# Kernel optimization log

Hardware: AMD Instinct MI355X
Metric: run time of the kernel (lower is better)

The kernel has to match this reference:

```python
import jax, jax.numpy as jnp
import numpy as np

B, T, C, H = 4, 2048, 1024, 16
DH = C // H  # 64


def setup_inputs() -> dict:
    key = jax.random.key(0)
    k_x, k_qkv, k_proj = jax.random.split(key, 3)
    x = jax.random.normal(k_x, (B, T, C), dtype=jnp.float32)
    # variance-scaling (fan_in) init for linear weights, torch layout [out, in]
    qkv_w = jax.random.normal(k_qkv, (3 * C, C), dtype=jnp.float32) * (1.0 / np.sqrt(C))
    qkv_b = jnp.zeros((3 * C,), dtype=jnp.float32)
    proj_w = jax.random.normal(k_proj, (C, C), dtype=jnp.float32) * (1.0 / np.sqrt(C))
    proj_b = jnp.zeros((C,), dtype=jnp.float32)
    # causal mask, broadcastable to [B, H, T, T]
    mask = jnp.tril(jnp.ones((T, T), dtype=bool))[None, None]
    return {"x": x, "qkv_w": qkv_w, "qkv_b": qkv_b,
            "proj_w": proj_w, "proj_b": proj_b, "mask": mask}


def reference(x, qkv_w, qkv_b, proj_w, proj_b, mask):
    b, t, c = x.shape
    scale = DH ** -0.5
    qkv = (x @ qkv_w.T + qkv_b).reshape(b, t, 3, H, DH)
    qkv = jnp.transpose(qkv, (2, 0, 3, 1, 4))  # [3, B, H, T, DH]
    q, k, v = qkv[0], qkv[1], qkv[2]
    attn = jnp.einsum("bhqd,bhkd->bhqk", q, k) * scale  # [B, H, T, T]
    neg = -jnp.finfo(attn.dtype).max
    attn = jnp.where(mask, attn, neg)
    attn = jax.nn.softmax(attn, axis=-1)
    out = jnp.einsum("bhqk,bhkd->bhqd", attn, v)  # [B, H, T, DH]
    out = jnp.transpose(out, (0, 2, 1, 3)).reshape(b, t, c)
    return out @ proj_w.T + proj_b
```

## Files before the change

### kernel.cpp

```cpp
#include <hip/hip_runtime.h>
#include <hip/hip_bf16.h>
#include <stdint.h>

#define B_ 4
#define T_ 2048
#define C_ 1024
#define H_ 16
#define DH_ 64
#define M_ (B_*T_)
#define NQKV_ (3*C_)
#define K_ C_

typedef __attribute__((ext_vector_type(8))) short short8;
typedef __attribute__((ext_vector_type(4))) float f32x4;
typedef __attribute__((ext_vector_type(4))) unsigned short us4;

union BFC { __hip_bfloat16 h; unsigned short u; };
__device__ inline unsigned short f2b(float f){ BFC c; c.h = __float2bfloat16(f); return c.u; }

__device__ inline void gload_lds16(const void* g, void* l){
  __builtin_amdgcn_global_load_lds(
    (const __attribute__((address_space(1))) void*)(uintptr_t)g,
    (__attribute__((address_space(3))) void*)(uintptr_t)l,
    16, 0, 0);
}

__global__ void cvt_f32_bf16(const float* __restrict__ src,
                             __hip_bfloat16* __restrict__ dst, int n4)
{
  int i = blockIdx.x * blockDim.x + threadIdx.x;
  int stride = gridDim.x * blockDim.x;
  for (; i < n4; i += stride) {
    float4 v = reinterpret_cast<const float4*>(src)[i];
    us4 o;
    o.x = f2b(v.x); o.y = f2b(v.y); o.z = f2b(v.z); o.w = f2b(v.w);
    reinterpret_cast<us4*>(dst)[i] = o;
  }
}

__global__ __launch_bounds__(512) void gemm_bt(
    const __hip_bfloat16* __restrict__ A,
    const __hip_bfloat16* __restrict__ Bw,
    const float* __restrict__ bias,
    int mode, int nbx,
    __hip_bfloat16* __restrict__ qdst,
    __hip_bfloat16* __restrict__ kdst,
    __hip_bfloat16* __restrict__ vdst,
    float* __restrict__ fdst)
{
  __shared__ char a_lds[2][32768];
  __shared__ char b_lds[2][32768];

  const int tid = threadIdx.x;
  const int lane = tid & 63;
  const int w = tid >> 6;
  const int l15 = lane & 15;
  const int lhi = lane >> 4;
  const int wm = w >> 2, wn = w & 3;

  const int nwg = gridDim.x;
  const int q8 = nwg >> 3;
  const int lb = (blockIdx.x & 7) * q8 + (blockIdx.x >> 3);
  const int bx = lb % nbx, by = lb / nbx;
  const int row0 = by * 256;
  const int col0 = bx * 256;

  int srow[4], scol[4];
#pragma unroll
  for (int i = 0; i < 4; ++i) {
    int L = i * 8192 + tid * 16;
    int r = L >> 7;
    int cb = (L & 127) ^ ((r & 7) << 4);
    srow[i] = r;
    scol[i] = cb >> 1;
  }

  const f32x4 zf = {0.f, 0.f, 0.f, 0.f};
  f32x4 acc[8][4];
#pragma unroll
  for (int m = 0; m < 8; ++m)
#pragma unroll
    for (int n = 0; n < 4; ++n) acc[m][n] = zf;

  const short* Ag = (const short*)A;
  const short* Bg = (const short*)Bw;

#define STAGE(kt, buf)                                                          \
  do {                                                                          \
    _Pragma("unroll")                                                           \
    for (int i = 0; i < 4; ++i) {                                               \
      gload_lds16(Ag + (size_t)(row0 + srow[i]) * K_ + (kt) + scol[i],          \
                  &a_lds[buf][i * 8192 + tid * 16]);                            \
      gload_lds16(Bg + (size_t)(col0 + srow[i]) * K_ + (kt) + scol[i],          \
                  &b_lds[buf][i * 8192 + tid * 16]);                            \
    }                                                                           \
  } while (0)

  STAGE(0, 0);
  __syncthreads();

  const int NKT = K_ / 64;
  for (int ki = 0; ki < NKT; ++ki) {
    const int cur = ki & 1;
    if (ki + 1 < NKT) STAGE((ki + 1) * 64, cur ^ 1);

#pragma unroll
    for (int kf = 0; kf < 2; ++kf) {
      short8 af[8], bfr[4];
#pragma unroll
      for (int m = 0; m < 8; ++m) {
        int r = wm * 128 + m * 16 + l15;
        af[m] = *(const short8*)(&a_lds[cur][r * 128 +
                     ((kf * 64 + lhi * 16) ^ ((r & 7) << 4))]);
      }
#pragma unroll
      for (int n = 0; n < 4; ++n) {
        int r = wn * 64 + n * 16 + l15;
        bfr[n] = *(const short8*)(&b_lds[cur][r * 128 +
                     ((kf * 64 + lhi * 16) ^ ((r & 7) << 4))]);
      }
#pragma unroll
      for (int m = 0; m < 8; ++m)
#pragma unroll
        for (int n = 0; n < 4; ++n)
          acc[m][n] = __builtin_amdgcn_mfma_f32_16x16x32_bf16(af[m], bfr[n],
                                                              acc[m][n], 0, 0, 0);
    }

    __syncthreads();
  }
#undef STAGE

  if (mode == 0) {
#pragma unroll
    for (int m = 0; m < 8; ++m) {
#pragma unroll
      for (int r = 0; r < 4; ++r) {
        int grow = row0 + wm * 128 + m * 16 + lhi * 4 + r;
        int b = grow >> 11, tt = grow & 2047;
#pragma unroll
        for (int n = 0; n < 4; ++n) {
          int gcol = col0 + wn * 64 + n * 16 + l15;
          float v = acc[m][n][r] + bias[gcol];
          int sel = gcol >> 10;
          int c1 = gcol & 1023;
          int hh = c1 >> 6, dh = c1 & 63;
          __hip_bfloat16 bv = __float2bfloat16(v);
          if (sel == 0)
            qdst[(((size_t)(b * H_ + hh)) * T_ + tt) * DH_ + dh] = bv;
          else if (sel == 1)
            kdst[(((size_t)(b * H_ + hh)) * T_ + tt) * DH_ + dh] = bv;
          else
            vdst[(((size_t)(b * H_ + hh)) * DH_ + dh) * T_ + tt] = bv;
        }
      }
    }
  } else {
#pragma unroll
    for (int m = 0; m < 8; ++m) {
#pragma unroll
      for (int r = 0; r < 4; ++r) {
        int grow = row0 + wm * 128 + m * 16 + lhi * 4 + r;
#pragma unroll
        for (int n = 0; n < 4; ++n) {
          int gcol = col0 + wn * 64 + n * 16 + l15;
          fdst[(size_t)grow * C_ + gcol] = acc[m][n][r] + bias[gcol];
        }
      }
    }
  }
}

__global__ __launch_bounds__(512, 2) void attn_kernel(
    const __hip_bfloat16* __restrict__ qg,
    const __hip_bfloat16* __restrict__ kg,
    const __hip_bfloat16* __restrict__ vtg,
    __hip_bfloat16* __restrict__ og)
{
  __shared__ char k_lds[2][8192];
  __shared__ char v_lds[2][8192];
  __shared__ char p_lds[8][4096];

  const int tid = threadIdx.x;
  const int lane = tid & 63;
  const int w = tid >> 6;
  const int l15 = lane & 15;
  const int lhi = lane >> 4;
  const int blk = blockIdx.x;
  const int bh = blk & 63;
  const int g = blk >> 6;
  const int qb = (g < 4) ? g : 11 - g;
  const int qr0 = qb * 256 + w * 32;
  const int nt = 4 * (qb + 1);
  const int tmask = qr0 >> 6;

  const char* kpb = (const char*)(kg + (size_t)bh * T_ * DH_);
  const char* vtpb = (const char*)(vtg + (size_t)bh * DH_ * T_);
  const short* qp = (const short*)(qg + (size_t)bh * T_ * DH_);
  char* pwl = p_lds[w];

  const int srow = tid >> 3;
  const int scb = ((tid & 7) << 4) ^ ((srow & 7) << 4);
  const int sdst = tid * 16;

  short8 qf[2][2];
#pragma unroll
  for (int m = 0; m < 2; ++m)
#pragma unroll
    for (int kf = 0; kf < 2; ++kf)
      qf[m][kf] = *(const short8*)(qp + (size_t)(qr0 + m * 16 + l15) * DH_ +
                                   kf * 32 + lhi * 8);

  const f32x4 zf = {0.f, 0.f, 0.f, 0.f};
  f32x4 o[2][4];
  float lsum[2][4];
#pragma unroll
  for (int m = 0; m < 2; ++m) {
#pragma unroll
    for (int n = 0; n < 4; ++n) o[m][n] = zf;
#pragma unroll
    for (int r = 0; r < 4; ++r) lsum[m][r] = 0.f;
  }

  gload_lds16(kpb + (size_t)srow * 128 + scb, &k_lds[0][sdst]);
  gload_lds16(vtpb + (size_t)srow * 4096 + scb, &v_lds[0][sdst]);
  __syncthreads();

  for (int t = 0; t < nt; ++t) {
    const int cur = t & 1;
    if (t + 1 < nt) {
      const int kv1 = (t + 1) * 64;
      gload_lds16(kpb + (size_t)(kv1 + srow) * 128 + scb, &k_lds[cur ^ 1][sdst]);
      gload_lds16(vtpb + (size_t)srow * 4096 + kv1 * 2 + scb, &v_lds[cur ^ 1][sdst]);
    }

    if (t <= tmask) {
      const int kv0 = t * 64;

      short8 kfr[2][4];
#pragma unroll
      for (int kf = 0; kf < 2; ++kf)
#pragma unroll
        for (int n = 0; n < 4; ++n) {
          int kr = n * 16 + l15;
          kfr[kf][n] = *(const short8*)(&k_lds[cur][kr * 128 +
                           ((kf * 64 + lhi * 16) ^ ((kr & 7) << 4))]);
        }

      f32x4 s[2][4];
#pragma unroll
      for (int m = 0; m < 2; ++m)
#pragma unroll
        for (int n = 0; n < 4; ++n) s[m][n] = zf;
#pragma unroll
      for (int kf = 0; kf < 2; ++kf)
#pragma unroll
        for (int n = 0; n < 4; ++n)
#pragma unroll
          for (int m = 0; m < 2; ++m)
            s[m][n] = __builtin_amdgcn_mfma_f32_16x16x32_bf16(qf[m][kf], kfr[kf][n],
                                                              s[m][n], 0, 0, 0);

      short8 vfr[2][4];
#pragma unroll
      for (int kf = 0; kf < 2; ++kf)
#pragma unroll
        for (int n = 0; n < 4; ++n) {
          int vr = n * 16 + l15;
          vfr[kf][n] = *(const short8*)(&v_lds[cur][vr * 128 +
                           ((kf * 64 + lhi * 16) ^ ((vr & 7) << 4))]);
        }

      if (t == tmask) {
#pragma unroll
        for (int m = 0; m < 2; ++m)
#pragma unroll
          for (int n = 0; n < 4; ++n)
#pragma unroll
            for (int r = 0; r < 4; ++r) {
              int kvA = kv0 + n * 16 + l15;
              int qA = qr0 + m * 16 + lhi * 4 + r;
              if (kvA > qA) s[m][n][r] = -1e30f;
            }
      }

#pragma unroll
      for (int m = 0; m < 2; ++m)
#pragma unroll
        for (int n = 0; n < 4; ++n)
#pragma unroll
          for (int r = 0; r < 4; ++r) {
            float pe = __expf(s[m][n][r] * 0.125f);
            s[m][n][r] = pe;
            lsum[m][r] += pe;
          }

#pragma unroll
      for (int m = 0; m < 2; ++m)
#pragma unroll
        for (int n = 0; n < 4; ++n)
#pragma unroll
          for (int r = 0; r < 4; ++r) {
            int row = m * 16 + lhi * 4 + r;
            *(unsigned short*)(pwl + row * 128 +
                               (((n * 16 + l15) * 2) ^ ((row & 7) << 4))) =
                f2b(s[m][n][r]);
          }
      short8 pa[2][2];
#pragma unroll
      for (int m = 0; m < 2; ++m)
#pragma unroll
        for (int kf = 0; kf < 2; ++kf) {
          int row = m * 16 + l15;
          pa[m][kf] = *(const short8*)(pwl + row * 128 +
                                       ((kf * 64 + lhi * 16) ^ ((row & 7) << 4)));
        }

#pragma unroll
      for (int kf = 0; kf < 2; ++kf)
#pragma unroll
        for (int n = 0; n < 4; ++n)
#pragma unroll
          for (int m = 0; m < 2; ++m)
            o[m][n] = __builtin_amdgcn_mfma_f32_16x16x32_bf16(pa[m][kf], vfr[kf][n],
                                                              o[m][n], 0, 0, 0);
    }

    __syncthreads();
  }

#pragma unroll
  for (int m = 0; m < 2; ++m)
#pragma unroll
    for (int r = 0; r < 4; ++r)
#pragma unroll
      for (int d = 1; d < 16; d <<= 1)
        lsum[m][r] += __shfl_xor(lsum[m][r], d, 64);

  const int b = bh >> 4, hd = bh & 15;
#pragma unroll
  for (int m = 0; m < 2; ++m)
#pragma unroll
    for (int r = 0; r < 4; ++r) {
      float inv = 1.f / lsum[m][r];
      int qrow = qr0 + m * 16 + lhi * 4 + r;
      __hip_bfloat16* orow = og + ((size_t)(b * T_ + qrow)) * C_ + hd * DH_;
#pragma unroll
      for (int n = 0; n < 4; ++n)
        orow[n * 16 + l15] = __float2bfloat16(o[m][n][r] * inv);
    }
}

extern "C" void kernel_launch(void* const* d_in, const int* in_sizes, int n_in,
                              void* d_out, int out_size, void* d_ws, size_t ws_size,
                              hipStream_t stream) {
  const float* x      = (const float*)d_in[0];
  const float* qkv_w  = (const float*)d_in[1];
  const float* qkv_b  = (const float*)d_in[2];
  const float* proj_w = (const float*)d_in[3];
  const float* proj_b = (const float*)d_in[4];
  float* out = (float*)d_out;

  char* ws = (char*)d_ws;
  __hip_bfloat16* xb    = (__hip_bfloat16*)(ws);
  __hip_bfloat16* wqkv  = (__hip_bfloat16*)(ws + 16777216);
  __hip_bfloat16* wproj = (__hip_bfloat16*)(ws + 23068672);
  __hip_bfloat16* qb    = (__hip_bfloat16*)(ws + 25165824);
  __hip_bfloat16* kb    = (__hip_bfloat16*)(ws + 41943040);
  __hip_bfloat16* vtb   = (__hip_bfloat16*)(ws + 58720256);
  __hip_bfloat16* att   = (__hip_bfloat16*)(ws + 75497472);

  cvt_f32_bf16<<<2048, 256, 0, stream>>>(x, xb, M_ * K_ / 4);
  cvt_f32_bf16<<<1024, 256, 0, stream>>>(qkv_w, wqkv, NQKV_ * K_ / 4);
  cvt_f32_bf16<<<512, 256, 0, stream>>>(proj_w, wproj, C_ * K_ / 4);

  gemm_bt<<<dim3((NQKV_/256) * (M_/256)), 512, 0, stream>>>(
      xb, wqkv, qkv_b, 0, NQKV_/256, qb, kb, vtb, nullptr);

  attn_kernel<<<dim3(512), 512, 0, stream>>>(qb, kb, vtb, att);

  gemm_bt<<<dim3((C_/256) * (M_/256)), 512, 0, stream>>>(
      att, wproj, proj_b, 1, C_/256, nullptr, nullptr, nullptr, out);
}
```

Before: 200.9 us.

## Deepen GEMM K-loop pipeline to four-stage ring with K=32 tiles

Splits the GEMM K tiles from 64 down to 32 and replaces the double buffer with a 4-slot LDS ring kept three stages ahead. Loads are waited on with explicit vmcnt counts and a raw s_barrier instead of a full __syncthreads. It also raises wave priority around the MFMA block. The aim is to hide global-load latency better and drop the second barrier per iteration, at the cost of more loop iterations and fragile hand-counted waitcnt logic.

```diff
diff --git a/kernel.cpp b/kernel.cpp
--- a/kernel.cpp
+++ b/kernel.cpp
@@ -48,8 +48,8 @@
     __hip_bfloat16* __restrict__ vdst,
     float* __restrict__ fdst)
 {
-  __shared__ char a_lds[2][32768];
-  __shared__ char b_lds[2][32768];
+  __shared__ char a_lds[4][16384];
+  __shared__ char b_lds[4][16384];
 
   const int tid = threadIdx.x;
   const int lane = tid & 63;
@@ -65,12 +65,12 @@
   const int row0 = by * 256;
   const int col0 = bx * 256;
 
-  int srow[4], scol[4];
-#pragma unroll
-  for (int i = 0; i < 4; ++i) {
+  int srow[2], scol[2];
+#pragma unroll
+  for (int i = 0; i < 2; ++i) {
     int L = i * 8192 + tid * 16;
-    int r = L >> 7;
-    int cb = (L & 127) ^ ((r & 7) << 4);
+    int r = L >> 6;
+    int cb = (L & 63) ^ ((r & 3) << 4);
     srow[i] = r;
     scol[i] = cb >> 1;
   }
@@ -85,49 +85,52 @@
   const short* Ag = (const short*)A;
   const short* Bg = (const short*)Bw;
 
-#define STAGE(kt, buf)                                                          \
+#define STAGE(kt, q)                                                            \
   do {                                                                          \
     _Pragma("unroll")                                                           \
-    for (int i = 0; i < 4; ++i) {                                               \
-      gload_lds16(Ag + (size_t)(row0 + srow[i]) * K_ + (kt) + scol[i],          \
-                  &a_lds[buf][i * 8192 + tid * 16]);                            \
-      gload_lds16(Bg + (size_t)(col0 + srow[i]) * K_ + (kt) + scol[i],          \
-                  &b_lds[buf][i * 8192 + tid * 16]);                            \
+    for (int i = 0; i < 2; ++i) {                                               \
+      gload_lds16(Ag + (size_t)(row0 + srow[i]) * K_ + (kt) * 32 + scol[i],     \
+                  &a_lds[q][i * 8192 + tid * 16]);                              \
+      gload_lds16(Bg + (size_t)(col0 + srow[i]) * K_ + (kt) * 32 + scol[i],     \
+                  &b_lds[q][i * 8192 + tid * 16]);                              \
     }                                                                           \
   } while (0)
 
   STAGE(0, 0);
-  __syncthreads();
-
-  const int NKT = K_ / 64;
-  for (int ki = 0; ki < NKT; ++ki) {
-    const int cur = ki & 1;
-    if (ki + 1 < NKT) STAGE((ki + 1) * 64, cur ^ 1);
-
-#pragma unroll
-    for (int kf = 0; kf < 2; ++kf) {
-      short8 af[8], bfr[4];
-#pragma unroll
-      for (int m = 0; m < 8; ++m) {
-        int r = wm * 128 + m * 16 + l15;
-        af[m] = *(const short8*)(&a_lds[cur][r * 128 +
-                     ((kf * 64 + lhi * 16) ^ ((r & 7) << 4))]);
-      }
-#pragma unroll
-      for (int n = 0; n < 4; ++n) {
-        int r = wn * 64 + n * 16 + l15;
-        bfr[n] = *(const short8*)(&b_lds[cur][r * 128 +
-                     ((kf * 64 + lhi * 16) ^ ((r & 7) << 4))]);
-      }
-#pragma unroll
-      for (int m = 0; m < 8; ++m)
-#pragma unroll
-        for (int n = 0; n < 4; ++n)
-          acc[m][n] = __builtin_amdgcn_mfma_f32_16x16x32_bf16(af[m], bfr[n],
-                                                              acc[m][n], 0, 0, 0);
-    }
-
-    __syncthreads();
+  STAGE(1, 1);
+  STAGE(2, 2);
+
+  const int NKT = K_ / 32;
+#pragma unroll 4
+  for (int kt = 0; kt < NKT; ++kt) {
+    const int q = kt & 3;
+    if (kt < NKT - 2)       asm volatile("s_waitcnt vmcnt(8)" ::: "memory");
+    else if (kt == NKT - 2) asm volatile("s_waitcnt vmcnt(4)" ::: "memory");
+    else                    asm volatile("s_waitcnt vmcnt(0)" ::: "memory");
+    __builtin_amdgcn_s_barrier();
+
+    if (kt + 3 < NKT) STAGE(kt + 3, (kt + 3) & 3);
+
+    short8 af[8], bfr[4];
+#pragma unroll
+    for (int m = 0; m < 8; ++m) {
+      int r = wm * 128 + m * 16 + l15;
+      af[m] = *(const short8*)(&a_lds[q][r * 64 + ((lhi * 16) ^ ((r & 3) << 4))]);
+    }
+#pragma unroll
+    for (int n = 0; n < 4; ++n) {
+      int r = wn * 64 + n * 16 + l15;
+      bfr[n] = *(const short8*)(&b_lds[q][r * 64 + ((lhi * 16) ^ ((r & 3) << 4))]);
+    }
+
+    __builtin_amdgcn_s_setprio(1);
+#pragma unroll
+    for (int m = 0; m < 8; ++m)
+#pragma unroll
+      for (int n = 0; n < 4; ++n)
+        acc[m][n] = __builtin_amdgcn_mfma_f32_16x16x32_bf16(af[m], bfr[n],
+                                                            acc[m][n], 0, 0, 0);
+    __builtin_amdgcn_s_setprio(0);
   }
 #undef STAGE
 
```

New measurement: 212.7 us. +5.9%, slower.

## Interleave GEMM LDS staging with MFMA phases and prefetch B two tiles ahead

Applied to the files above, without the earlier changes.

Restructures the GEMM main loop into four phases per K-tile. Each phase loads a slice of A fragments, issues part of the next tile's global-to-LDS copies, and runs MFMAs at raised wave priority. B is staged two tiles ahead into the buffer being consumed, using explicit vmcnt waits and barriers. The goal is to overlap global loads with compute and replace the single end-of-tile sync with finer-grained scheduling. In exchange it adds more barriers per tile and relies on delicate manual waitcnt accounting, where an error could cause races.

```diff
diff --git a/kernel.cpp b/kernel.cpp
--- a/kernel.cpp
+++ b/kernel.cpp
@@ -85,51 +85,79 @@
   const short* Ag = (const short*)A;
   const short* Bg = (const short*)Bw;
 
-#define STAGE(kt, buf)                                                          \
-  do {                                                                          \
-    _Pragma("unroll")                                                           \
-    for (int i = 0; i < 4; ++i) {                                               \
-      gload_lds16(Ag + (size_t)(row0 + srow[i]) * K_ + (kt) + scol[i],          \
-                  &a_lds[buf][i * 8192 + tid * 16]);                            \
-      gload_lds16(Bg + (size_t)(col0 + srow[i]) * K_ + (kt) + scol[i],          \
-                  &b_lds[buf][i * 8192 + tid * 16]);                            \
-    }                                                                           \
-  } while (0)
-
-  STAGE(0, 0);
-  __syncthreads();
+#define STG_A(kt, buf, i)                                                      \
+  gload_lds16(Ag + (size_t)(row0 + srow[i]) * K_ + (kt) * 64 + scol[i],        \
+              &a_lds[buf][(i) * 8192 + tid * 16])
+#define STG_B(kt, buf, i)                                                      \
+  gload_lds16(Bg + (size_t)(col0 + srow[i]) * K_ + (kt) * 64 + scol[i],        \
+              &b_lds[buf][(i) * 8192 + tid * 16])
+
+#define MFMA_(a, b, c) __builtin_amdgcn_mfma_f32_16x16x32_bf16(a, b, c, 0, 0, 0)
+
+#define PHASE(q, STG)                                                          \
+  {                                                                            \
+    short8 a00, a01, a10, a11;                                                 \
+    { int r = wm * 128 + (2 * (q)) * 16 + l15;                                 \
+      int base = r * 128, swz = (r & 7) << 4;                                  \
+      a00 = *(const short8*)(&a_lds[cur][base + ((lhi * 16) ^ swz)]);          \
+      a01 = *(const short8*)(&a_lds[cur][base + ((64 + lhi * 16) ^ swz)]); }   \
+    { int r = wm * 128 + (2 * (q) + 1) * 16 + l15;                             \
+      int base = r * 128, swz = (r & 7) << 4;                                  \
+      a10 = *(const short8*)(&a_lds[cur][base + ((lhi * 16) ^ swz)]);          \
+      a11 = *(const short8*)(&a_lds[cur][base + ((64 + lhi * 16) ^ swz)]); }   \
+    STG;                                                                       \
+    __builtin_amdgcn_sched_barrier(0);                                         \
+    __builtin_amdgcn_s_barrier();                                              \
+    asm volatile("s_waitcnt lgkmcnt(0)" ::: "memory");                         \
+    __builtin_amdgcn_sched_barrier(0);                                         \
+    __builtin_amdgcn_s_setprio(1);                                             \
+    _Pragma("unroll")                                                          \
+    for (int n = 0; n < 4; ++n) {                                              \
+      acc[2 * (q)][n]     = MFMA_(a00, bq0[n], acc[2 * (q)][n]);               \
+      acc[2 * (q)][n]     = MFMA_(a01, bq1[n], acc[2 * (q)][n]);               \
+      acc[2 * (q) + 1][n] = MFMA_(a10, bq0[n], acc[2 * (q) + 1][n]);           \
+      acc[2 * (q) + 1][n] = MFMA_(a11, bq1[n], acc[2 * (q) + 1][n]);           \
+    }                                                                          \
+    __builtin_amdgcn_s_setprio(0);                                             \
+    __builtin_amdgcn_sched_barrier(0);                                         \
+  }
+
+  STG_B(0, 0, 0); STG_B(0, 0, 1); STG_B(0, 0, 2); STG_B(0, 0, 3);
+  STG_A(0, 0, 0); STG_A(0, 0, 1); STG_A(0, 0, 2); STG_A(0, 0, 3);
+  STG_B(1, 1, 0); STG_B(1, 1, 1); STG_B(1, 1, 2); STG_B(1, 1, 3);
+  asm volatile("s_waitcnt vmcnt(4)" ::: "memory");
+  __builtin_amdgcn_sched_barrier(0);
+  __builtin_amdgcn_s_barrier();
 
   const int NKT = K_ / 64;
-  for (int ki = 0; ki < NKT; ++ki) {
-    const int cur = ki & 1;
-    if (ki + 1 < NKT) STAGE((ki + 1) * 64, cur ^ 1);
-
-#pragma unroll
-    for (int kf = 0; kf < 2; ++kf) {
-      short8 af[8], bfr[4];
-#pragma unroll
-      for (int m = 0; m < 8; ++m) {
-        int r = wm * 128 + m * 16 + l15;
-        af[m] = *(const short8*)(&a_lds[cur][r * 128 +
-                     ((kf * 64 + lhi * 16) ^ ((r & 7) << 4))]);
-      }
-#pragma unroll
-      for (int n = 0; n < 4; ++n) {
-        int r = wn * 64 + n * 16 + l15;
-        bfr[n] = *(const short8*)(&b_lds[cur][r * 128 +
-                     ((kf * 64 + lhi * 16) ^ ((r & 7) << 4))]);
-      }
-#pragma unroll
-      for (int m = 0; m < 8; ++m)
-#pragma unroll
-        for (int n = 0; n < 4; ++n)
-          acc[m][n] = __builtin_amdgcn_mfma_f32_16x16x32_bf16(af[m], bfr[n],
-                                                              acc[m][n], 0, 0, 0);
-    }
-
-    __syncthreads();
-  }
-#undef STAGE
+  for (int t = 0; t < NKT; ++t) {
+    const int cur = t & 1;
+    const int nxt = cur ^ 1;
+
+    short8 bq0[4], bq1[4];
+#pragma unroll
+    for (int n = 0; n < 4; ++n) {
+      int rb = wn * 64 + n * 16 + l15;
+      int base = rb * 128, swz = (rb & 7) << 4;
+      bq0[n] = *(const short8*)(&b_lds[cur][base + ((lhi * 16) ^ swz)]);
+      bq1[n] = *(const short8*)(&b_lds[cur][base + ((64 + lhi * 16) ^ swz)]);
+    }
+
+    PHASE(0, if (t + 1 < NKT) { STG_A(t + 1, nxt, 0); STG_A(t + 1, nxt, 1); });
+    __builtin_amdgcn_s_barrier();
+    PHASE(1, if (t + 1 < NKT) { STG_A(t + 1, nxt, 2); STG_A(t + 1, nxt, 3); });
+    __builtin_amdgcn_s_barrier();
+    PHASE(2, if (t + 2 < NKT) { STG_B(t + 2, cur, 0); STG_B(t + 2, cur, 1); });
+    __builtin_amdgcn_s_barrier();
+    PHASE(3, if (t + 2 < NKT) { STG_B(t + 2, cur, 2); STG_B(t + 2, cur, 3); });
+    if (t < NKT - 1) asm volatile("s_waitcnt vmcnt(4)" ::: "memory");
+    else             asm volatile("s_waitcnt vmcnt(0)" ::: "memory");
+    __builtin_amdgcn_sched_barrier(0);
+    __builtin_amdgcn_s_barrier();
+  }
+#undef PHASE
+#undef STG_A
+#undef STG_B
 
   if (mode == 0) {
 #pragma unroll
```

Measured after the change: 204.2 us. Within noise of the previous version (+1.6%).
